# Kernel optimization log

Measured on AMD Instinct MI355X. Metric: run time of the kernel, lower is better.

## Reference

```python
import jax, jax.numpy as jnp
import numpy as np

B, H, F, G = 32768, 256, 32, 16
N = F * G * 2  # total number of heads


def setup_inputs() -> dict:
    key = jax.random.key(0)
    kx, kw, kb = jax.random.split(key, 3)
    x = jax.random.normal(kx, (B, H), dtype=jnp.float32)
    # stacked weights/biases of all N = in_features*granularity*2 Linear(H,1) heads
    W = jax.random.normal(kw, (N, H), dtype=jnp.float32) * (1.0 / jnp.sqrt(H))
    b = jax.random.normal(kb, (N,), dtype=jnp.float32) * 0.01
    return {"x": x, "W": W, "b": b}


def reference(x, W, b):
    # Fused equivalent of N independent Linear(H,1)+Sigmoid heads:
    # one [B,H] x [H,N] matmul + bias + sigmoid, then reshape to [B,F,G,2].
    z = jax.nn.sigmoid(jnp.einsum("bh,nh->bn", x, W) + b)
    return z.reshape(x.shape[0], F, G, 2)
```

## Files before the change

kernel.cpp:

```cpp
#include <hip/hip_runtime.h>
#include <hip/hip_fp16.h>

typedef _Float16 half8 __attribute__((ext_vector_type(8)));
typedef float floatx4 __attribute__((ext_vector_type(4)));

#define KH 256
#define NN 1024
#define BM 64
#define STN 64
#define NST (NN / STN)
#define ST_F16 (STN * KH)

__global__ __launch_bounds__(256)
void pack_w(const float* __restrict__ W, _Float16* __restrict__ P) {
    const int u  = blockIdx.x * 256 + threadIdx.x;
    const int g  = u >> 9;
    const int ks = (u >> 6) & 7;
    const int l  = u & 63;
    const int n  = g * 16 + (l & 15);
    const int kb = ks * 32 + ((l >> 4) << 3);
    const float* src = W + (size_t)n * KH + kb;
    floatx4 lo = *(const floatx4*)src;
    floatx4 hi = *(const floatx4*)(src + 4);
    half8 h;
    h[0] = (_Float16)lo[0]; h[1] = (_Float16)lo[1];
    h[2] = (_Float16)lo[2]; h[3] = (_Float16)lo[3];
    h[4] = (_Float16)hi[0]; h[5] = (_Float16)hi[1];
    h[6] = (_Float16)hi[2]; h[7] = (_Float16)hi[3];
    *(half8*)(P + (size_t)u * 8) = h;
}

__global__ __launch_bounds__(256, 2)
void lfh_main(const float* __restrict__ x, const _Float16* __restrict__ P,
              const float* __restrict__ bias, float* __restrict__ out) {
    __shared__ _Float16 Ws[2][ST_F16];

    const int t   = threadIdx.x;
    const int w   = t >> 6;
    const int l   = t & 63;
    const int l15 = l & 15;
    const int lq  = l >> 4;
    const int m0  = blockIdx.x * BM;
    const int brow = m0 + w * 16 + l15;

    half8 afrag[8];
    {
        const float* xr = x + (size_t)brow * KH;
        #pragma unroll
        for (int ks = 0; ks < 8; ++ks) {
            const int kb = ks * 32 + lq * 8;
            floatx4 lo = *(const floatx4*)(xr + kb);
            floatx4 hi = *(const floatx4*)(xr + kb + 4);
            half8 f;
            f[0] = (_Float16)lo[0]; f[1] = (_Float16)lo[1];
            f[2] = (_Float16)lo[2]; f[3] = (_Float16)lo[3];
            f[4] = (_Float16)hi[0]; f[5] = (_Float16)hi[1];
            f[6] = (_Float16)hi[2]; f[7] = (_Float16)hi[3];
            afrag[ks] = f;
        }
    }

    auto stage = [&](int st, _Float16* dst) {
        const _Float16* gsrc = P + (size_t)st * ST_F16;
        #pragma unroll
        for (int r = 0; r < 8; ++r) {
            __builtin_amdgcn_global_load_lds(
                (const __attribute__((address_space(1))) void*)(gsrc + r * 2048 + t * 8),
                (__attribute__((address_space(3))) void*)(dst + r * 2048 + t * 8),
                16, 0, 0);
        }
    };

    stage(0, Ws[0]);
    __syncthreads();

    int cur = 0;
    for (int st = 0; st < NST; ++st) {
        if (st + 1 < NST) stage(st + 1, Ws[cur ^ 1]);

        const _Float16* Bt = Ws[cur];
        #pragma unroll
        for (int nf = 0; nf < 4; ++nf) {
            floatx4 acc = (floatx4)0.0f;
            #pragma unroll
            for (int ks = 0; ks < 8; ++ks) {
                half8 wf = *(const half8*)(Bt + ((nf * 8 + ks) * 64 + l) * 8);
                acc = __builtin_amdgcn_mfma_f32_16x16x32_f16(wf, afrag[ks], acc, 0, 0, 0);
            }
            const int nb = st * STN + nf * 16 + lq * 4;
            floatx4 bv = *(const floatx4*)(bias + nb);
            floatx4 r;
            #pragma unroll
            for (int j = 0; j < 4; ++j) {
                const float z = acc[j] + bv[j];
                r[j] = __builtin_amdgcn_rcpf(1.0f + __expf(-z));
            }
            __builtin_nontemporal_store(r, (floatx4*)(out + (size_t)brow * NN + nb));
        }
        __syncthreads();
        cur ^= 1;
    }
}

extern "C" void kernel_launch(void* const* d_in, const int* in_sizes, int n_in,
                              void* d_out, int out_size, void* d_ws, size_t ws_size,
                              hipStream_t stream) {
    const float* x = (const float*)d_in[0];
    const float* W = (const float*)d_in[1];
    const float* b = (const float*)d_in[2];
    float* out = (float*)d_out;
    _Float16* P = (_Float16*)d_ws;

    pack_w<<<dim3(128), dim3(256), 0, stream>>>(W, P);

    const int Btot = in_sizes[0] / KH;
    lfh_main<<<dim3(Btot / BM), dim3(256), 0, stream>>>(x, P, b, out);
}
```

Baseline: 51.75 us.

## Drop LDS staging of weights, read fragments from global, split N across grid

Removes the double-buffered LDS staging of packed fp16 weights. Each lane now loads its weight fragments straight from global memory (L2/L1-cached) and the output columns are split across a second grid dimension, which doubles block count and raises the occupancy hint to 4. The aim is to cut LDS traffic and syncthreads overhead and to improve latency hiding. In exchange, x is loaded and converted twice, once per split, and every wave issues global loads for weights that were shared through LDS before.

After: 72.49 us. 1.4x slower.

```diff
diff --git a/kernel.cpp b/kernel.cpp
--- a/kernel.cpp
+++ b/kernel.cpp
@@ -7,9 +7,9 @@
 #define KH 256
 #define NN 1024
 #define BM 64
-#define STN 64
-#define NST (NN / STN)
-#define ST_F16 (STN * KH)
+#define NSPLIT 2
+#define NG (NN / 16)
+#define GPB (NG / NSPLIT)
 
 __global__ __launch_bounds__(256)
 void pack_w(const float* __restrict__ W, _Float16* __restrict__ P) {
@@ -30,18 +30,16 @@
     *(half8*)(P + (size_t)u * 8) = h;
 }
 
-__global__ __launch_bounds__(256, 2)
+__global__ __launch_bounds__(256, 4)
 void lfh_main(const float* __restrict__ x, const _Float16* __restrict__ P,
               const float* __restrict__ bias, float* __restrict__ out) {
-    __shared__ _Float16 Ws[2][ST_F16];
-
     const int t   = threadIdx.x;
     const int w   = t >> 6;
     const int l   = t & 63;
     const int l15 = l & 15;
     const int lq  = l >> 4;
-    const int m0  = blockIdx.x * BM;
-    const int brow = m0 + w * 16 + l15;
+    const int brow = blockIdx.x * BM + w * 16 + l15;
+    const int g0   = blockIdx.y * GPB;
 
     half8 afrag[8];
     {
@@ -60,34 +58,21 @@
         }
     }
 
-    auto stage = [&](int st, _Float16* dst) {
-        const _Float16* gsrc = P + (size_t)st * ST_F16;
-        #pragma unroll
-        for (int r = 0; r < 8; ++r) {
-            __builtin_amdgcn_global_load_lds(
-                (const __attribute__((address_space(1))) void*)(gsrc + r * 2048 + t * 8),
-                (__attribute__((address_space(3))) void*)(dst + r * 2048 + t * 8),
-                16, 0, 0);
-        }
-    };
+    float* orow = out + (size_t)brow * NN;
+    const _Float16* Pl = P + (size_t)l * 8;
 
-    stage(0, Ws[0]);
-    __syncthreads();
-
-    int cur = 0;
-    for (int st = 0; st < NST; ++st) {
-        if (st + 1 < NST) stage(st + 1, Ws[cur ^ 1]);
-
-        const _Float16* Bt = Ws[cur];
+    for (int gg = 0; gg < GPB; gg += 4) {
         #pragma unroll
         for (int nf = 0; nf < 4; ++nf) {
+            const int g = g0 + gg + nf;
+            const _Float16* fb = Pl + (size_t)g * 4096;
             floatx4 acc = (floatx4)0.0f;
             #pragma unroll
             for (int ks = 0; ks < 8; ++ks) {
-                half8 wf = *(const half8*)(Bt + ((nf * 8 + ks) * 64 + l) * 8);
+                half8 wf = *(const half8*)(fb + ks * 512);
                 acc = __builtin_amdgcn_mfma_f32_16x16x32_f16(wf, afrag[ks], acc, 0, 0, 0);
             }
-            const int nb = st * STN + nf * 16 + lq * 4;
+            const int nb = g * 16 + lq * 4;
             floatx4 bv = *(const floatx4*)(bias + nb);
             floatx4 r;
             #pragma unroll
@@ -95,10 +80,9 @@
                 const float z = acc[j] + bv[j];
                 r[j] = __builtin_amdgcn_rcpf(1.0f + __expf(-z));
             }
-            __builtin_nontemporal_store(r, (floatx4*)(out + (size_t)brow * NN + nb));
+            __builtin_nontemporal_store(r, (floatx4*)(orow + nb));
         }
-        __syncthreads();
-        cur ^= 1;
+        __builtin_amdgcn_s_barrier();
     }
 }
 
@@ -114,5 +98,5 @@
     pack_w<<<dim3(128), dim3(256), 0, stream>>>(W, P);
 
     const int Btot = in_sizes[0] / KH;
-    lfh_main<<<dim3(Btot / BM), dim3(256), 0, stream>>>(x, P, b, out);
+    lfh_main<<<dim3(Btot / BM, NSPLIT), dim3(256), 0, stream>>>(x, P, b, out);
 }
```
